# Kernel tuning notes

Measured on AMD Instinct MI355X. Metric: run time of the kernel, lower is better.

## Reference

```python
import jax, jax.numpy as jnp
import numpy as np

# NF4 codebook (QLoRA): 16 quantile values of a standard normal, normalized to [-1, 1]
NF4_TABLE = jnp.array([
    -1.0, -0.6961928009986877, -0.5250730514526367, -0.39491748809814453,
    -0.28444138169288635, -0.18477343022823334, -0.09105003625154495, 0.0,
    0.07958029955625534, 0.16093020141124725, 0.24611230194568634,
    0.33791524171829224, 0.44070982933044434, 0.5626170039176941,
    0.7229568362236328, 1.0], dtype=jnp.float32)

IN_DIM = 4096
OUT_DIM = 4096
RANK = 16
ALPHA = 32.0
BLOCK = 64  # NF4 quantization block size along the flattened weight


def setup_inputs() -> dict:
    key = jax.random.key(0)
    k1, k2, k3, k4, k5 = jax.random.split(key, 5)
    x = jax.random.normal(k1, (4, 2048, IN_DIM), dtype=jnp.float32)
    # 4-bit codes into NF4_TABLE, stored unpacked as int32
    w_codes = jax.random.randint(k2, (OUT_DIM, IN_DIM), 0, 16, dtype=jnp.int32)
    # per-block absmax scales (positive)
    w_scales = jax.random.uniform(k3, (OUT_DIM, IN_DIM // BLOCK), dtype=jnp.float32) * 0.02 + 1e-3
    # lora_a: kaiming-uniform-ish scale; lora_b: nonzero for testability (original inits to zeros)
    lora_a = jax.random.normal(k4, (RANK, IN_DIM), dtype=jnp.float32) * (1.0 / np.sqrt(IN_DIM))
    lora_b = jax.random.normal(k5, (OUT_DIM, RANK), dtype=jnp.float32) * 0.01
    return {"x": x, "w_codes": w_codes, "w_scales": w_scales, "lora_a": lora_a, "lora_b": lora_b}


def _dequant_nf4(w_codes, w_scales):
    # codes [O, I] -> dequantized weight [O, I]
    w = NF4_TABLE[w_codes]                                   # [O, I]
    w = w.reshape(OUT_DIM, IN_DIM // BLOCK, BLOCK) * w_scales[:, :, None]
    return w.reshape(OUT_DIM, IN_DIM)


def reference(x, w_codes, w_scales, lora_a, lora_b):
    # base: frozen NF4 linear (dequantize then matmul), no bias
    w = _dequant_nf4(w_codes, w_scales)                      # [O, I]
    base = jnp.einsum('bsi,oi->bso', x, w)                   # [B, S, O]
    # LoRA path: dropout p=0.0 -> identity; scale alpha / rank
    ax = jnp.einsum('bsi,ri->bsr', x, lora_a)                # [B, S, r]
    lora = jnp.einsum('bsr,or->bso', ax, lora_b)             # [B, S, O]
    return base + (ALPHA / RANK) * lora
```

## Files before the change

kernel.cpp:

```cpp
#include <hip/hip_runtime.h>
#include <hip/hip_bf16.h>


#define IN_DIM  4096
#define OUT_DIM 4096
#define RANK    16
#define M_TOK   8192
#define LORA_SCALE 2.0f

typedef __bf16 bf16_t;
typedef bf16_t bf16x8 __attribute__((ext_vector_type(8)));
typedef float  f32x4  __attribute__((ext_vector_type(4)));

__device__ __constant__ float NF4_TAB[16] = {
    -1.0f, -0.6961928009986877f, -0.5250730514526367f, -0.39491748809814453f,
    -0.28444138169288635f, -0.18477343022823334f, -0.09105003625154495f, 0.0f,
    0.07958029955625534f, 0.16093020141124725f, 0.24611230194568634f,
    0.33791524171829224f, 0.44070982933044434f, 0.5626170039176941f,
    0.7229568362236328f, 1.0f};

__global__ __launch_bounds__(256) void prep_w(
    const int* __restrict__ codes, const float* __restrict__ scales,
    const float* __restrict__ la, const float* __restrict__ lb,
    bf16_t* __restrict__ W)
{
    __shared__ float nf4s[16];
    __shared__ float lbs[4][16];
    const int o0 = blockIdx.x * 4;
    const int tid = threadIdx.x;
    if (tid < 64) lbs[tid >> 4][tid & 15] = lb[(o0 + (tid >> 4)) * RANK + (tid & 15)] * LORA_SCALE;
    else if (tid < 80) nf4s[tid - 64] = NF4_TAB[tid - 64];
    __syncthreads();

    #pragma unroll
    for (int it = 0; it < 2; ++it) {
        const int i0 = (it * 256 + tid) * 8;
        float w[4][8];
        #pragma unroll
        for (int oo = 0; oo < 4; ++oo) {
            const size_t base = (size_t)(o0 + oo) * IN_DIM + i0;
            int4 c0 = *(const int4*)(codes + base);
            int4 c1 = *(const int4*)(codes + base + 4);
            const float sc = scales[(o0 + oo) * (IN_DIM / 64) + (i0 >> 6)];
            w[oo][0] = nf4s[c0.x] * sc; w[oo][1] = nf4s[c0.y] * sc;
            w[oo][2] = nf4s[c0.z] * sc; w[oo][3] = nf4s[c0.w] * sc;
            w[oo][4] = nf4s[c1.x] * sc; w[oo][5] = nf4s[c1.y] * sc;
            w[oo][6] = nf4s[c1.z] * sc; w[oo][7] = nf4s[c1.w] * sc;
        }
        #pragma unroll
        for (int r = 0; r < RANK; ++r) {
            float4 a0 = *(const float4*)(la + r * IN_DIM + i0);
            float4 a1 = *(const float4*)(la + r * IN_DIM + i0 + 4);
            #pragma unroll
            for (int oo = 0; oo < 4; ++oo) {
                const float b = lbs[oo][r];
                w[oo][0] += b * a0.x; w[oo][1] += b * a0.y;
                w[oo][2] += b * a0.z; w[oo][3] += b * a0.w;
                w[oo][4] += b * a1.x; w[oo][5] += b * a1.y;
                w[oo][6] += b * a1.z; w[oo][7] += b * a1.w;
            }
        }
        #pragma unroll
        for (int oo = 0; oo < 4; ++oo) {
            bf16x8 v;
            #pragma unroll
            for (int j = 0; j < 8; ++j) v[j] = (bf16_t)w[oo][j];
            *(bf16x8*)(W + (size_t)(o0 + oo) * IN_DIM + i0) = v;
        }
    }
}

__global__ __launch_bounds__(256) void cast_x(
    const float* __restrict__ x, bf16_t* __restrict__ y, int n8)
{
    const int stride = gridDim.x * blockDim.x;
    for (int i = blockIdx.x * blockDim.x + threadIdx.x; i < n8; i += stride) {
        const size_t e = (size_t)i * 8;
        float4 a = *(const float4*)(x + e);
        float4 b = *(const float4*)(x + e + 4);
        bf16x8 v;
        v[0] = (bf16_t)a.x; v[1] = (bf16_t)a.y; v[2] = (bf16_t)a.z; v[3] = (bf16_t)a.w;
        v[4] = (bf16_t)b.x; v[5] = (bf16_t)b.y; v[6] = (bf16_t)b.z; v[7] = (bf16_t)b.w;
        *(bf16x8*)(y + e) = v;
    }
}

__global__ __launch_bounds__(512, 2) void gemm_bt(
    const bf16_t* __restrict__ A, const bf16_t* __restrict__ B,
    float* __restrict__ C)
{
    __shared__ __align__(128) char lds[131072];

    const int tid  = threadIdx.x;
    const int wave = tid >> 6;
    const int lane = tid & 63;

    const int flat = blockIdx.y * gridDim.x + blockIdx.x;
    const int swz  = (flat & 7) * 64 + (flat >> 3);
    const int bx = swz & 15;
    const int by = swz >> 4;
    const int m0 = by * 256;
    const int n0 = bx * 256;

    const int wr = wave >> 2;
    const int wc = wave & 3;

    f32x4 acc[8][4];
    #pragma unroll
    for (int i = 0; i < 8; ++i)
        #pragma unroll
        for (int j = 0; j < 4; ++j) acc[i][j] = (f32x4)0.0f;

    const int frow = lane & 15;
    const int fch  = lane >> 4;
    const int fxor = (fch ^ ((frow >> 1) & 3)) << 4;
    const int aoff = (wr * 128 + frow) * 64 + fxor;
    const int boff = (wc * 64  + frow) * 64 + fxor;

    const int d0 = tid * 16, d1 = 8192 + tid * 16;
    const int sr0 = d0 >> 6, sr1 = d1 >> 6;
    const int sg0 = ((d0 >> 4) & 3) ^ ((sr0 >> 1) & 3);
    const int sg1 = ((d1 >> 4) & 3) ^ ((sr1 >> 1) & 3);
    const char* gA = (const char*)A;
    const char* gB = (const char*)B;

    bf16x8 fAe[8], fAo[8], fBe[2], fBo[2];

#define RD_A(FA, SL, KH) do {                                                  \
    const char* b_ = lds + (SL) * 65536 + (KH) * 16384;                        \
    _Pragma("unroll")                                                          \
    for (int f_ = 0; f_ < 8; ++f_)                                             \
        FA[f_] = *(const bf16x8*)(b_ + aoff + f_ * 1024);                      \
} while (0)

#define RD_B(FB, SL, KH, NH) do {                                              \
    const char* b_ = lds + (SL) * 65536 + 32768 + (KH) * 16384;                \
    FB[0] = *(const bf16x8*)(b_ + boff + (NH) * 2048);                         \
    FB[1] = *(const bf16x8*)(b_ + boff + (NH) * 2048 + 1024);                  \
} while (0)

#define STG1(OPI, KH_, SL, T) do {                                             \
    const char* g_  = (OPI) ? gB : gA;                                         \
    const int   r0_ = (OPI) ? n0 : m0;                                         \
    const size_t ko_ = (size_t)(T) * 128 + (KH_) * 64;                         \
    const char* s0_ = g_ + (size_t)(r0_ + sr0) * 8192 + ko_ + (sg0 << 4);      \
    const char* s1_ = g_ + (size_t)(r0_ + sr1) * 8192 + ko_ + (sg1 << 4);      \
    char* db_ = lds + (SL) * 65536 + (OPI) * 32768 + (KH_) * 16384 + wave * 1024; \
    __builtin_amdgcn_global_load_lds(                                          \
        (const __attribute__((address_space(1))) void*)s0_,                    \
        (__attribute__((address_space(3))) void*)db_, 16, 0, 0);               \
    __builtin_amdgcn_global_load_lds(                                          \
        (const __attribute__((address_space(1))) void*)s1_,                    \
        (__attribute__((address_space(3))) void*)(db_ + 8192), 16, 0, 0);      \
} while (0)

#define MM(FA, FB, NH) do {                                                    \
    __builtin_amdgcn_s_setprio(1);                                             \
    _Pragma("unroll")                                                          \
    for (int f_ = 0; f_ < 8; ++f_) {                                           \
        acc[f_][(NH)*2+0] = __builtin_amdgcn_mfma_f32_16x16x32_bf16(           \
            FA[f_], FB[0], acc[f_][(NH)*2+0], 0, 0, 0);                        \
        acc[f_][(NH)*2+1] = __builtin_amdgcn_mfma_f32_16x16x32_bf16(           \
            FA[f_], FB[1], acc[f_][(NH)*2+1], 0, 0, 0);                        \
    }                                                                          \
    __builtin_amdgcn_s_setprio(0);                                             \
} while (0)

#define PHASE(SOP, SKH, SSL, ST, CHK, FA, FB, NH, ...) do {                    \
    __VA_ARGS__;                                                               \
    STG1(SOP, SKH, SSL, ST);                                                   \
    if (CHK) { asm volatile("s_waitcnt vmcnt(8)" ::: "memory"); }              \
    __builtin_amdgcn_sched_barrier(0);                                         \
    __builtin_amdgcn_s_barrier();                                              \
    MM(FA, FB, NH);                                                            \
    __builtin_amdgcn_s_barrier();                                              \
} while (0)

    STG1(0, 0, 0, 0); STG1(1, 0, 0, 0); STG1(0, 1, 0, 0); STG1(1, 1, 0, 0);
    STG1(0, 0, 1, 1); STG1(1, 0, 1, 1); STG1(0, 1, 1, 1);
    asm volatile("s_waitcnt vmcnt(6)" ::: "memory");
    __builtin_amdgcn_s_barrier();
    RD_A(fAe, 0, 0); RD_B(fBe, 0, 0, 0);

    for (int i = 0; i < 32; ++i) {
        const int tS0 = (2 * i + 2) & 63;
        const int tS1 = (2 * i + 3) & 63;
        const int tY  = (2 * i + 1) & 63;
        PHASE(1, 1, 1, tY,  1, fAe, fBe, 0, RD_B(fBo, 0, 0, 1));
        PHASE(0, 0, 0, tS0, 0, fAe, fBo, 1, RD_A(fAo, 0, 1); RD_B(fBe, 0, 1, 0));
        PHASE(1, 0, 0, tS0, 1, fAo, fBe, 0, RD_B(fBo, 0, 1, 1));
        PHASE(0, 1, 0, tS0, 0, fAo, fBo, 1, RD_A(fAe, 1, 0); RD_B(fBe, 1, 0, 0));
        PHASE(1, 1, 0, tS0, 1, fAe, fBe, 0, RD_B(fBo, 1, 0, 1));
        PHASE(0, 0, 1, tS1, 0, fAe, fBo, 1, RD_A(fAo, 1, 1); RD_B(fBe, 1, 1, 0));
        PHASE(1, 0, 1, tS1, 1, fAo, fBe, 0, RD_B(fBo, 1, 1, 1));
        PHASE(0, 1, 1, tS1, 0, fAo, fBo, 1, RD_A(fAe, 0, 0); RD_B(fBe, 0, 0, 0));
    }

    const int crow = (lane >> 4) * 4;
    const int ccol = lane & 15;
    #pragma unroll
    for (int i = 0; i < 8; ++i) {
        #pragma unroll
        for (int j = 0; j < 4; ++j) {
            const int mb = m0 + wr * 128 + i * 16 + crow;
            const int nb = n0 + wc * 64 + j * 16 + ccol;
            #pragma unroll
            for (int r = 0; r < 4; ++r)
                C[(size_t)(mb + r) * OUT_DIM + nb] = acc[i][j][r];
        }
    }
#undef RD_A
#undef RD_B
#undef STG1
#undef MM
#undef PHASE
}

extern "C" void kernel_launch(void* const* d_in, const int* in_sizes, int n_in,
                              void* d_out, int out_size, void* d_ws, size_t ws_size,
                              hipStream_t stream) {
    const float* x      = (const float*)d_in[0];
    const int*   codes  = (const int*)d_in[1];
    const float* scales = (const float*)d_in[2];
    const float* la     = (const float*)d_in[3];
    const float* lb     = (const float*)d_in[4];
    float* out = (float*)d_out;

    bf16_t* W  = (bf16_t*)d_ws;
    bf16_t* xb = (bf16_t*)((char*)d_ws + (size_t)OUT_DIM * IN_DIM * 2);

    prep_w<<<OUT_DIM / 4, 256, 0, stream>>>(codes, scales, la, lb, W);
    cast_x<<<2048, 256, 0, stream>>>(x, xb, (M_TOK * IN_DIM) / 8);

    dim3 grid(OUT_DIM / 256, M_TOK / 256);
    gemm_bt<<<grid, 512, 0, stream>>>(xb, W, out);
}
```

Measured before the change: 298.4 us.

## Interleave LDS fragment reads between MFMA groups inside each GEMM phase

Splits each phase's 16 MFMAs into four groups of four and places the LDS fragment reads for the next phase between them, rather than issuing all reads before the barrier. A-fragment loads are spread over two phases so LDS latency overlaps matrix math. The waitcnt placement and vmcnt threshold move to match the new load ordering. This raises register pressure and carries a risk of a hazard if the wait thresholds are not exactly right.

```diff
diff --git a/kernel.cpp b/kernel.cpp
--- a/kernel.cpp
+++ b/kernel.cpp
@@ -126,11 +126,10 @@
 
     bf16x8 fAe[8], fAo[8], fBe[2], fBo[2];
 
-#define RD_A(FA, SL, KH) do {                                                  \
+#define RD_A2(FA, SL, KH, J0) do {                                             \
     const char* b_ = lds + (SL) * 65536 + (KH) * 16384;                        \
-    _Pragma("unroll")                                                          \
-    for (int f_ = 0; f_ < 8; ++f_)                                             \
-        FA[f_] = *(const bf16x8*)(b_ + aoff + f_ * 1024);                      \
+    FA[(J0)]     = *(const bf16x8*)(b_ + aoff + (J0) * 1024);                  \
+    FA[(J0) + 1] = *(const bf16x8*)(b_ + aoff + ((J0) + 1) * 1024);            \
 } while (0)
 
 #define RD_B(FB, SL, KH, NH) do {                                              \
@@ -154,25 +153,28 @@
         (__attribute__((address_space(3))) void*)(db_ + 8192), 16, 0, 0);      \
 } while (0)
 
-#define MM(FA, FB, NH) do {                                                    \
-    __builtin_amdgcn_s_setprio(1);                                             \
+#define MM4(FA, F0, FB, BI, NH) do {                                           \
     _Pragma("unroll")                                                          \
-    for (int f_ = 0; f_ < 8; ++f_) {                                           \
-        acc[f_][(NH)*2+0] = __builtin_amdgcn_mfma_f32_16x16x32_bf16(           \
-            FA[f_], FB[0], acc[f_][(NH)*2+0], 0, 0, 0);                        \
-        acc[f_][(NH)*2+1] = __builtin_amdgcn_mfma_f32_16x16x32_bf16(           \
-            FA[f_], FB[1], acc[f_][(NH)*2+1], 0, 0, 0);                        \
-    }                                                                          \
-    __builtin_amdgcn_s_setprio(0);                                             \
-} while (0)
-
-#define PHASE(SOP, SKH, SSL, ST, CHK, FA, FB, NH, ...) do {                    \
-    __VA_ARGS__;                                                               \
+    for (int f_ = 0; f_ < 4; ++f_)                                             \
+        acc[(F0) + f_][(NH) * 2 + (BI)] =                                      \
+            __builtin_amdgcn_mfma_f32_16x16x32_bf16(                           \
+                FA[(F0) + f_], FB[BI], acc[(F0) + f_][(NH) * 2 + (BI)], 0, 0, 0); \
+} while (0)
+
+#define PHASE(SOP, SKH, SSL, ST, CHK, FA, FB, NH, RD1, RD2, RD3) do {          \
     STG1(SOP, SKH, SSL, ST);                                                   \
-    if (CHK) { asm volatile("s_waitcnt vmcnt(8)" ::: "memory"); }              \
+    if (CHK) { asm volatile("s_waitcnt vmcnt(6)" ::: "memory"); }              \
     __builtin_amdgcn_sched_barrier(0);                                         \
     __builtin_amdgcn_s_barrier();                                              \
-    MM(FA, FB, NH);                                                            \
+    __builtin_amdgcn_s_setprio(1);                                             \
+    MM4(FA, 0, FB, 0, NH);                                                     \
+    RD1;                                                                       \
+    MM4(FA, 0, FB, 1, NH);                                                     \
+    RD2;                                                                       \
+    MM4(FA, 4, FB, 0, NH);                                                     \
+    RD3;                                                                       \
+    MM4(FA, 4, FB, 1, NH);                                                     \
+    __builtin_amdgcn_s_setprio(0);                                             \
     __builtin_amdgcn_s_barrier();                                              \
 } while (0)
 
@@ -180,20 +182,30 @@
     STG1(0, 0, 1, 1); STG1(1, 0, 1, 1); STG1(0, 1, 1, 1);
     asm volatile("s_waitcnt vmcnt(6)" ::: "memory");
     __builtin_amdgcn_s_barrier();
-    RD_A(fAe, 0, 0); RD_B(fBe, 0, 0, 0);
+    RD_A2(fAe, 0, 0, 0); RD_A2(fAe, 0, 0, 2);
+    RD_A2(fAe, 0, 0, 4); RD_A2(fAe, 0, 0, 6);
+    RD_B(fBe, 0, 0, 0);
 
     for (int i = 0; i < 32; ++i) {
+        const int tY  = 2 * i + 1;
         const int tS0 = (2 * i + 2) & 63;
         const int tS1 = (2 * i + 3) & 63;
-        const int tY  = (2 * i + 1) & 63;
-        PHASE(1, 1, 1, tY,  1, fAe, fBe, 0, RD_B(fBo, 0, 0, 1));
-        PHASE(0, 0, 0, tS0, 0, fAe, fBo, 1, RD_A(fAo, 0, 1); RD_B(fBe, 0, 1, 0));
-        PHASE(1, 0, 0, tS0, 1, fAo, fBe, 0, RD_B(fBo, 0, 1, 1));
-        PHASE(0, 1, 0, tS0, 0, fAo, fBo, 1, RD_A(fAe, 1, 0); RD_B(fBe, 1, 0, 0));
-        PHASE(1, 1, 0, tS0, 1, fAe, fBe, 0, RD_B(fBo, 1, 0, 1));
-        PHASE(0, 0, 1, tS1, 0, fAe, fBo, 1, RD_A(fAo, 1, 1); RD_B(fBe, 1, 1, 0));
-        PHASE(1, 0, 1, tS1, 1, fAo, fBe, 0, RD_B(fBo, 1, 1, 1));
-        PHASE(0, 1, 1, tS1, 0, fAo, fBo, 1, RD_A(fAe, 0, 0); RD_B(fBe, 0, 0, 0));
+        PHASE(1, 1, 1, tY,  0, fAe, fBe, 0,
+              RD_A2(fAo, 0, 1, 0), RD_A2(fAo, 0, 1, 2), RD_B(fBo, 0, 0, 1));
+        PHASE(0, 0, 0, tS0, 1, fAe, fBo, 1,
+              RD_A2(fAo, 0, 1, 4), RD_A2(fAo, 0, 1, 6), RD_B(fBe, 0, 1, 0));
+        PHASE(1, 0, 0, tS0, 0, fAo, fBe, 0,
+              RD_A2(fAe, 1, 0, 0), RD_A2(fAe, 1, 0, 2), RD_B(fBo, 0, 1, 1));
+        PHASE(0, 1, 0, tS0, 1, fAo, fBo, 1,
+              RD_A2(fAe, 1, 0, 4), RD_A2(fAe, 1, 0, 6), RD_B(fBe, 1, 0, 0));
+        PHASE(1, 1, 0, tS0, 0, fAe, fBe, 0,
+              RD_A2(fAo, 1, 1, 0), RD_A2(fAo, 1, 1, 2), RD_B(fBo, 1, 0, 1));
+        PHASE(0, 0, 1, tS1, 1, fAe, fBo, 1,
+              RD_A2(fAo, 1, 1, 4), RD_A2(fAo, 1, 1, 6), RD_B(fBe, 1, 1, 0));
+        PHASE(1, 0, 1, tS1, 0, fAo, fBe, 0,
+              RD_A2(fAe, 0, 0, 0), RD_A2(fAe, 0, 0, 2), RD_B(fBo, 1, 1, 1));
+        PHASE(0, 1, 1, tS1, 1, fAo, fBo, 1,
+              RD_A2(fAe, 0, 0, 4), RD_A2(fAe, 0, 0, 6), RD_B(fBe, 0, 0, 0));
     }
 
     const int crow = (lane >> 4) * 4;
@@ -209,10 +221,10 @@
                 C[(size_t)(mb + r) * OUT_DIM + nb] = acc[i][j][r];
         }
     }
-#undef RD_A
+#undef RD_A2
 #undef RD_B
 #undef STG1
-#undef MM
+#undef MM4
 #undef PHASE
 }
 
```

Result: no change. 293.7 us (-1.6%).

## Merge prep kernels and restructure GEMM LDS pipeline without fragment double-buffering

Applied to the files above, without the earlier changes.

Merges the weight dequant+LoRA-fold kernel and the x-to-bf16 cast kernel into one launch, with block index selecting the role. This removes a launch and lets both memory-bound passes share the GPU at once. In the GEMM main loop, it drops the even/odd register fragment double-buffering and reads each phase's fragments just before its MFMAs. Each phase now waits on lgkmcnt(0), and the prologue fully preloads both stages and waits on vmcnt(0). This lowers register pressure and simplifies the schedule, but it exposes LDS read latency before every MFMA block instead of hiding it behind the previous phase's compute.

```diff
diff --git a/kernel.cpp b/kernel.cpp
--- a/kernel.cpp
+++ b/kernel.cpp
@@ -19,69 +19,70 @@
     0.33791524171829224f, 0.44070982933044434f, 0.5626170039176941f,
     0.7229568362236328f, 1.0f};
 
-__global__ __launch_bounds__(256) void prep_w(
+__global__ __launch_bounds__(256) void prep_all(
+    const float* __restrict__ x,
     const int* __restrict__ codes, const float* __restrict__ scales,
     const float* __restrict__ la, const float* __restrict__ lb,
-    bf16_t* __restrict__ W)
+    bf16_t* __restrict__ W, bf16_t* __restrict__ xb)
 {
-    __shared__ float nf4s[16];
-    __shared__ float lbs[4][16];
-    const int o0 = blockIdx.x * 4;
     const int tid = threadIdx.x;
-    if (tid < 64) lbs[tid >> 4][tid & 15] = lb[(o0 + (tid >> 4)) * RANK + (tid & 15)] * LORA_SCALE;
-    else if (tid < 80) nf4s[tid - 64] = NF4_TAB[tid - 64];
-    __syncthreads();
-
-    #pragma unroll
-    for (int it = 0; it < 2; ++it) {
-        const int i0 = (it * 256 + tid) * 8;
-        float w[4][8];
+    if (blockIdx.x < 1024) {
+        __shared__ float nf4s[16];
+        __shared__ float lbs[4][16];
+        const int o0 = blockIdx.x * 4;
+        if (tid < 64) lbs[tid >> 4][tid & 15] = lb[(o0 + (tid >> 4)) * RANK + (tid & 15)] * LORA_SCALE;
+        else if (tid < 80) nf4s[tid - 64] = NF4_TAB[tid - 64];
+        __syncthreads();
+
         #pragma unroll
-        for (int oo = 0; oo < 4; ++oo) {
-            const size_t base = (size_t)(o0 + oo) * IN_DIM + i0;
-            int4 c0 = *(const int4*)(codes + base);
-            int4 c1 = *(const int4*)(codes + base + 4);
-            const float sc = scales[(o0 + oo) * (IN_DIM / 64) + (i0 >> 6)];
-            w[oo][0] = nf4s[c0.x] * sc; w[oo][1] = nf4s[c0.y] * sc;
-            w[oo][2] = nf4s[c0.z] * sc; w[oo][3] = nf4s[c0.w] * sc;
-            w[oo][4] = nf4s[c1.x] * sc; w[oo][5] = nf4s[c1.y] * sc;
-            w[oo][6] = nf4s[c1.z] * sc; w[oo][7] = nf4s[c1.w] * sc;
-        }
-        #pragma unroll
-        for (int r = 0; r < RANK; ++r) {
-            float4 a0 = *(const float4*)(la + r * IN_DIM + i0);
-            float4 a1 = *(const float4*)(la + r * IN_DIM + i0 + 4);
+        for (int it = 0; it < 2; ++it) {
+            const int i0 = (it * 256 + tid) * 8;
+            float w[4][8];
             #pragma unroll
             for (int oo = 0; oo < 4; ++oo) {
-                const float b = lbs[oo][r];
-                w[oo][0] += b * a0.x; w[oo][1] += b * a0.y;
-                w[oo][2] += b * a0.z; w[oo][3] += b * a0.w;
-                w[oo][4] += b * a1.x; w[oo][5] += b * a1.y;
-                w[oo][6] += b * a1.z; w[oo][7] += b * a1.w;
+                const size_t base = (size_t)(o0 + oo) * IN_DIM + i0;
+                int4 c0 = *(const int4*)(codes + base);
+                int4 c1 = *(const int4*)(codes + base + 4);
+                const float sc = scales[(o0 + oo) * (IN_DIM / 64) + (i0 >> 6)];
+                w[oo][0] = nf4s[c0.x] * sc; w[oo][1] = nf4s[c0.y] * sc;
+                w[oo][2] = nf4s[c0.z] * sc; w[oo][3] = nf4s[c0.w] * sc;
+                w[oo][4] = nf4s[c1.x] * sc; w[oo][5] = nf4s[c1.y] * sc;
+                w[oo][6] = nf4s[c1.z] * sc; w[oo][7] = nf4s[c1.w] * sc;
+            }
+            #pragma unroll
+            for (int r = 0; r < RANK; ++r) {
+                float4 a0 = *(const float4*)(la + r * IN_DIM + i0);
+                float4 a1 = *(const float4*)(la + r * IN_DIM + i0 + 4);
+                #pragma unroll
+                for (int oo = 0; oo < 4; ++oo) {
+                    const float b = lbs[oo][r];
+                    w[oo][0] += b * a0.x; w[oo][1] += b * a0.y;
+                    w[oo][2] += b * a0.z; w[oo][3] += b * a0.w;
+                    w[oo][4] += b * a1.x; w[oo][5] += b * a1.y;
+                    w[oo][6] += b * a1.z; w[oo][7] += b * a1.w;
+                }
+            }
+            #pragma unroll
+            for (int oo = 0; oo < 4; ++oo) {
+                bf16x8 v;
+                #pragma unroll
+                for (int j = 0; j < 8; ++j) v[j] = (bf16_t)w[oo][j];
+                *(bf16x8*)(W + (size_t)(o0 + oo) * IN_DIM + i0) = v;
             }
         }
-        #pragma unroll
-        for (int oo = 0; oo < 4; ++oo) {
+    } else {
+        const int bid = blockIdx.x - 1024;
+        const int n8 = (M_TOK * IN_DIM) / 8;
+        const int stride = 2048 * 256;
+        for (int i = bid * 256 + tid; i < n8; i += stride) {
+            const size_t e = (size_t)i * 8;
+            float4 a = *(const float4*)(x + e);
+            float4 b = *(const float4*)(x + e + 4);
             bf16x8 v;
-            #pragma unroll
-            for (int j = 0; j < 8; ++j) v[j] = (bf16_t)w[oo][j];
-            *(bf16x8*)(W + (size_t)(o0 + oo) * IN_DIM + i0) = v;
+            v[0] = (bf16_t)a.x; v[1] = (bf16_t)a.y; v[2] = (bf16_t)a.z; v[3] = (bf16_t)a.w;
+            v[4] = (bf16_t)b.x; v[5] = (bf16_t)b.y; v[6] = (bf16_t)b.z; v[7] = (bf16_t)b.w;
+            *(bf16x8*)(xb + e) = v;
         }
-    }
-}
-
-__global__ __launch_bounds__(256) void cast_x(
-    const float* __restrict__ x, bf16_t* __restrict__ y, int n8)
-{
-    const int stride = gridDim.x * blockDim.x;
-    for (int i = blockIdx.x * blockDim.x + threadIdx.x; i < n8; i += stride) {
-        const size_t e = (size_t)i * 8;
-        float4 a = *(const float4*)(x + e);
-        float4 b = *(const float4*)(x + e + 4);
-        bf16x8 v;
-        v[0] = (bf16_t)a.x; v[1] = (bf16_t)a.y; v[2] = (bf16_t)a.z; v[3] = (bf16_t)a.w;
-        v[4] = (bf16_t)b.x; v[5] = (bf16_t)b.y; v[6] = (bf16_t)b.z; v[7] = (bf16_t)b.w;
-        *(bf16x8*)(y + e) = v;
     }
 }
 
@@ -124,19 +125,19 @@
     const char* gA = (const char*)A;
     const char* gB = (const char*)B;
 
-    bf16x8 fAe[8], fAo[8], fBe[2], fBo[2];
-
-#define RD_A(FA, SL, KH) do {                                                  \
+    bf16x8 fA[8], fB[2];
+
+#define RD_A8(SL, KH) do {                                                     \
     const char* b_ = lds + (SL) * 65536 + (KH) * 16384;                        \
     _Pragma("unroll")                                                          \
     for (int f_ = 0; f_ < 8; ++f_)                                             \
-        FA[f_] = *(const bf16x8*)(b_ + aoff + f_ * 1024);                      \
-} while (0)
-
-#define RD_B(FB, SL, KH, NH) do {                                              \
+        fA[f_] = *(const bf16x8*)(b_ + aoff + f_ * 1024);                      \
+} while (0)
+
+#define RD_B2(SL, KH, NH) do {                                                 \
     const char* b_ = lds + (SL) * 65536 + 32768 + (KH) * 16384;                \
-    FB[0] = *(const bf16x8*)(b_ + boff + (NH) * 2048);                         \
-    FB[1] = *(const bf16x8*)(b_ + boff + (NH) * 2048 + 1024);                  \
+    fB[0] = *(const bf16x8*)(b_ + boff + (NH) * 2048);                         \
+    fB[1] = *(const bf16x8*)(b_ + boff + (NH) * 2048 + 1024);                  \
 } while (0)
 
 #define STG1(OPI, KH_, SL, T) do {                                             \
@@ -154,46 +155,46 @@
         (__attribute__((address_space(3))) void*)(db_ + 8192), 16, 0, 0);      \
 } while (0)
 
-#define MM(FA, FB, NH) do {                                                    \
+#define MM16(NH) do {                                                          \
     __builtin_amdgcn_s_setprio(1);                                             \
     _Pragma("unroll")                                                          \
     for (int f_ = 0; f_ < 8; ++f_) {                                           \
-        acc[f_][(NH)*2+0] = __builtin_amdgcn_mfma_f32_16x16x32_bf16(           \
-            FA[f_], FB[0], acc[f_][(NH)*2+0], 0, 0, 0);                        \
-        acc[f_][(NH)*2+1] = __builtin_amdgcn_mfma_f32_16x16x32_bf16(           \
-            FA[f_], FB[1], acc[f_][(NH)*2+1], 0, 0, 0);                        \
+        acc[f_][(NH) * 2 + 0] = __builtin_amdgcn_mfma_f32_16x16x32_bf16(       \
+            fA[f_], fB[0], acc[f_][(NH) * 2 + 0], 0, 0, 0);                    \
+        acc[f_][(NH) * 2 + 1] = __builtin_amdgcn_mfma_f32_16x16x32_bf16(       \
+            fA[f_], fB[1], acc[f_][(NH) * 2 + 1], 0, 0, 0);                    \
     }                                                                          \
     __builtin_amdgcn_s_setprio(0);                                             \
 } while (0)
 
-#define PHASE(SOP, SKH, SSL, ST, CHK, FA, FB, NH, ...) do {                    \
-    __VA_ARGS__;                                                               \
+#define PHASE(VM, SOP, SKH, SSL, ST, NH, RDS) do {                             \
+    if (VM) { asm volatile("s_waitcnt vmcnt(5)" ::: "memory"); }               \
+    RDS;                                                                       \
     STG1(SOP, SKH, SSL, ST);                                                   \
-    if (CHK) { asm volatile("s_waitcnt vmcnt(8)" ::: "memory"); }              \
+    __builtin_amdgcn_s_barrier();                                              \
+    asm volatile("s_waitcnt lgkmcnt(0)" ::: "memory");                         \
     __builtin_amdgcn_sched_barrier(0);                                         \
+    MM16(NH);                                                                  \
     __builtin_amdgcn_s_barrier();                                              \
-    MM(FA, FB, NH);                                                            \
-    __builtin_amdgcn_s_barrier();                                              \
 } while (0)
 
     STG1(0, 0, 0, 0); STG1(1, 0, 0, 0); STG1(0, 1, 0, 0); STG1(1, 1, 0, 0);
-    STG1(0, 0, 1, 1); STG1(1, 0, 1, 1); STG1(0, 1, 1, 1);
-    asm volatile("s_waitcnt vmcnt(6)" ::: "memory");
+    STG1(0, 0, 1, 1); STG1(1, 0, 1, 1); STG1(0, 1, 1, 1); STG1(1, 1, 1, 1);
+    asm volatile("s_waitcnt vmcnt(0)" ::: "memory");
     __builtin_amdgcn_s_barrier();
-    RD_A(fAe, 0, 0); RD_B(fBe, 0, 0, 0);
 
     for (int i = 0; i < 32; ++i) {
-        const int tS0 = (2 * i + 2) & 63;
-        const int tS1 = (2 * i + 3) & 63;
-        const int tY  = (2 * i + 1) & 63;
-        PHASE(1, 1, 1, tY,  1, fAe, fBe, 0, RD_B(fBo, 0, 0, 1));
-        PHASE(0, 0, 0, tS0, 0, fAe, fBo, 1, RD_A(fAo, 0, 1); RD_B(fBe, 0, 1, 0));
-        PHASE(1, 0, 0, tS0, 1, fAo, fBe, 0, RD_B(fBo, 0, 1, 1));
-        PHASE(0, 1, 0, tS0, 0, fAo, fBo, 1, RD_A(fAe, 1, 0); RD_B(fBe, 1, 0, 0));
-        PHASE(1, 1, 0, tS0, 1, fAe, fBe, 0, RD_B(fBo, 1, 0, 1));
-        PHASE(0, 0, 1, tS1, 0, fAe, fBo, 1, RD_A(fAo, 1, 1); RD_B(fBe, 1, 1, 0));
-        PHASE(1, 0, 1, tS1, 1, fAo, fBe, 0, RD_B(fBo, 1, 1, 1));
-        PHASE(0, 1, 1, tS1, 0, fAo, fBo, 1, RD_A(fAe, 0, 0); RD_B(fBe, 0, 0, 0));
+        const int tO  = (2 * i + 1) & 63;
+        const int tE2 = (2 * i + 2) & 63;
+        const int tO2 = (2 * i + 3) & 63;
+        PHASE(1, 1, 1, 1, tO,  0, RD_A8(0, 0); RD_B2(0, 0, 0));
+        PHASE(0, 0, 0, 0, tE2, 1, RD_B2(0, 0, 1));
+        PHASE(1, 1, 0, 0, tE2, 0, RD_A8(0, 1); RD_B2(0, 1, 0));
+        PHASE(0, 0, 1, 0, tE2, 1, RD_B2(0, 1, 1));
+        PHASE(1, 1, 1, 0, tE2, 0, RD_A8(1, 0); RD_B2(1, 0, 0));
+        PHASE(0, 0, 0, 1, tO2, 1, RD_B2(1, 0, 1));
+        PHASE(1, 1, 0, 1, tO2, 0, RD_A8(1, 1); RD_B2(1, 1, 0));
+        PHASE(0, 0, 1, 1, tO2, 1, RD_B2(1, 1, 1));
     }
 
     const int crow = (lane >> 4) * 4;
@@ -209,10 +210,10 @@
                 C[(size_t)(mb + r) * OUT_DIM + nb] = acc[i][j][r];
         }
     }
-#undef RD_A
-#undef RD_B
+#undef RD_A8
+#undef RD_B2
 #undef STG1
-#undef MM
+#undef MM16
 #undef PHASE
 }
 
@@ -229,8 +230,7 @@
     bf16_t* W  = (bf16_t*)d_ws;
     bf16_t* xb = (bf16_t*)((char*)d_ws + (size_t)OUT_DIM * IN_DIM * 2);
 
-    prep_w<<<OUT_DIM / 4, 256, 0, stream>>>(codes, scales, la, lb, W);
-    cast_x<<<2048, 256, 0, stream>>>(x, xb, (M_TOK * IN_DIM) / 8);
+    prep_all<<<1024 + 2048, 256, 0, stream>>>(x, codes, scales, la, lb, W, xb);
 
     dim3 grid(OUT_DIM / 256, M_TOK / 256);
     gemm_bt<<<grid, 512, 0, stream>>>(xb, W, out);
```

Result: no change. 297.6 us (-0.3%).
